# Kernel tuning notes

Measured on AMD Instinct MI355X. Metric: run time of the kernel, lower is better.

Reference implementation:

```python
import jax, jax.numpy as jnp
import numpy as np
from jax import lax

N_FFT = 2048
HOP = 512
N_ITER = 60
MOMENTUM = 0.99 / (1.0 + 0.99)  # torchaudio normalizes momentum/(1+momentum)
EPS = 1e-16
PAD = N_FFT // 2


def _hann(n):
    # periodic hann window, matches torch.hann_window(n)
    return 0.5 - 0.5 * jnp.cos(2.0 * jnp.pi * jnp.arange(n, dtype=jnp.float32) / n)


def _stft(x, window):
    # x: (B, L) real -> (B, F, T) complex. center=True, reflect pad, onesided, unnormalized.
    B, L = x.shape
    xp = jnp.pad(x, ((0, 0), (PAD, PAD)), mode='reflect')
    T = 1 + (L + 2 * PAD - N_FFT) // HOP
    idx = jnp.arange(T)[:, None] * HOP + jnp.arange(N_FFT)[None, :]  # (T, N)
    frames = xp[:, idx] * window  # (B, T, N)
    spec = jnp.fft.rfft(frames, axis=-1)  # (B, T, F)
    return jnp.swapaxes(spec, 1, 2)  # (B, F, T)


def _istft(spec, window):
    # spec: (B, F, T) complex -> (B, hop*(T-1)) real. Matches torch.istft(center=True).
    B, F, T = spec.shape
    frames = jnp.fft.irfft(jnp.swapaxes(spec, 1, 2), n=N_FFT, axis=-1) * window  # (B, T, N)
    L_pad = N_FFT + HOP * (T - 1)
    idx_flat = (jnp.arange(T)[:, None] * HOP + jnp.arange(N_FFT)[None, :]).reshape(-1)
    y = jnp.zeros((B, L_pad), frames.dtype).at[:, idx_flat].add(frames.reshape(B, -1))
    wsq = jnp.zeros((L_pad,), window.dtype).at[idx_flat].add(
        jnp.tile(window * window, T))
    y = y / jnp.where(wsq > 1e-11, wsq, 1.0)
    return y[:, PAD:L_pad - PAD]


def _griffin_lim(spec, window):
    # spec: (B, F, T) nonnegative magnitudes (power=1.0 so no pow needed)
    spec_c = spec.astype(jnp.complex64)
    angles0 = jnp.ones_like(spec_c)   # rand_init=False -> full of ones
    tprev0 = jnp.zeros_like(spec_c)

    def step(carry, _):
        angles, tprev = carry
        inv = _istft(spec_c * angles, window)
        rebuilt = _stft(inv, window)
        a = rebuilt - tprev * MOMENTUM
        a = a / (jnp.abs(a) + EPS)
        return (a, rebuilt), None

    (angles, _), _ = lax.scan(step, (angles0, tprev0), None, length=N_ITER)
    return _istft(spec_c * angles, window)


def setup_inputs() -> dict:
    key = jax.random.key(0)
    B, T, F = 4, 400, N_FFT // 2 + 1
    spectrogram = jax.random.uniform(key, (B, T, F), dtype=jnp.float32)
    return {"spectrogram": spectrogram}


def reference(spectrogram):
    window = _hann(N_FFT)
    spec = jnp.transpose(spectrogram, (0, 2, 1))  # (B, F, T)
    return _griffin_lim(spec, window)  # (B, HOP*(T-1))
```

## Files before the change

kernel.cpp:

```cpp
#include <hip/hip_runtime.h>
#include <math.h>

constexpr int BB   = 4;
constexpr int TT   = 400;
constexpr int FF   = 1025;
constexpr int NFFT = 2048;
constexpr int HOP  = 512;
constexpr int PADD = 1024;
constexpr int LL   = HOP * (TT - 1);
constexpr int LPAD = NFFT + HOP * (TT - 1);
constexpr int NITER = 60;
constexpr double MOM = 0.99 / 1.99;
constexpr double EPSV = 1e-16;
constexpr double DPI = 3.14159265358979323846;

constexpr size_t OFF_TW1024 = 0;
constexpr size_t OFF_TW2048 = 2048;
constexpr size_t OFF_TPR    = 4098;
constexpr size_t OFF_FRM    = 3284098;
constexpr size_t OFF_XP     = 6560898;
constexpr size_t OFF_WIN32  = 7386242;
constexpr size_t OFF_WSQ32  = 7387266;
constexpr size_t WS_DOUBLES = 7490434;

__device__ __forceinline__ double2 cmuld(double2 a, double2 b) {
    return make_double2(a.x * b.x - a.y * b.y, a.x * b.y + a.y * b.x);
}

__device__ __forceinline__ float np_cosf(float x) {
    const float rint_cvt = 0x1.800000p+23f;
    float qf = __builtin_fmaf(x, 0x1.45f306p-1f, rint_cvt) - rint_cvt;
    float r = __builtin_fmaf(qf, -0x1.921fb0p+0f, x);
    r = __builtin_fmaf(qf, -0x1.5110b4p-22f, r);
    r = __builtin_fmaf(qf, -0x1.846988p-48f, r);
    r = __builtin_fmaf(qf, -0x1.8cc966p-73f, r);
    int q = (int)qf + 1;
    float r2 = r * r;
    float cosp = __builtin_fmaf(0x1.98e616p-16f, r2, -0x1.6c06dcp-10f);
    cosp = __builtin_fmaf(cosp, r2, 0x1.55553cp-5f);
    cosp = __builtin_fmaf(cosp, r2, -0x1.000000p-1f);
    cosp = __builtin_fmaf(cosp, r2, 0x1.000000p+0f);
    float sinp = __builtin_fmaf(0x1.7d3bbcp-19f, r2, -0x1.a06bbap-13f);
    sinp = __builtin_fmaf(sinp, r2, 0x1.11119ap-7f);
    sinp = __builtin_fmaf(sinp, r2, -0x1.555548p-3f);
    sinp = sinp * r2;
    sinp = __builtin_fmaf(sinp, r, r);
    float res = (q & 1) ? cosp : sinp;
    return (q & 2) ? -res : res;
}

__global__ void k_init_tables(double2* tw1024, double2* tw2048, float* win) {
    int n = blockIdx.x * blockDim.x + threadIdx.x;
    if (n < 1024) {
        double th = -2.0 * DPI * (double)n / 1024.0;
        double s, c; sincos(th, &s, &c);
        tw1024[n] = make_double2(c, s);
    }
    if (n < 1025) {
        double th = -2.0 * DPI * (double)n / 2048.0;
        double s, c; sincos(th, &s, &c);
        tw2048[n] = make_double2(c, s);
    }
    if (n < 2048) {
        const float TWO_PI_F = 6.283185307179586f;
        float ang = __fdiv_rn(__fmul_rn(TWO_PI_F, (float)n), 2048.0f);
        float c = np_cosf(ang);
        win[n] = __fsub_rn(0.5f, __fmul_rn(0.5f, c));
    }
}

__global__ void k_init_wsq(const float* __restrict__ win, float* __restrict__ wsq) {
    int m = blockIdx.x * blockDim.x + threadIdx.x;
    if (m >= LPAD) return;
    int tlo = (m - (NFFT - HOP)) >> 9;
    if (tlo < 0) tlo = 0;
    int thi = m >> 9;
    if (thi > TT - 1) thi = TT - 1;
    float s = 0.0f;
    for (int t = tlo; t <= thi; ++t) {
        float w = win[m - (t << 9)];
        s = __fadd_rn(s, __fmul_rn(w, w));
    }
    wsq[m] = (s > 1e-11f) ? s : 1.0f;
}

__global__ void k_init_state(double2* __restrict__ tpr) {
    int i = blockIdx.x * blockDim.x + threadIdx.x;
    if (i < BB * TT * FF) tpr[i] = make_double2(0.0, 0.0);
}

template <int DIR>
__device__ void fft1024_w(double2* buf, const double2* __restrict__ tw, int tid) {
#pragma unroll
    for (int s = 0; s < 5; ++s) {
        const int p = 1 << (2 * s);
        double2 o0[4], o1[4], o2[4], o3[4];
        int jj[4];
#pragma unroll
        for (int q = 0; q < 4; ++q) {
            int v = tid + 64 * q;
            int k = v & (p - 1);
            jj[q] = ((v - k) << 2) + k;
            double2 a = buf[v];
            double2 b = buf[v + 256];
            double2 c = buf[v + 512];
            double2 d = buf[v + 768];
            int t1 = k << (8 - 2 * s);
            double2 w1 = tw[t1 & 1023];
            double2 w2 = tw[(2 * t1) & 1023];
            double2 w3 = tw[(3 * t1) & 1023];
            if (DIR > 0) { w1.y = -w1.y; w2.y = -w2.y; w3.y = -w3.y; }
            b = cmuld(b, w1);
            c = cmuld(c, w2);
            d = cmuld(d, w3);
            double2 u0 = make_double2(a.x + c.x, a.y + c.y);
            double2 u1 = make_double2(a.x - c.x, a.y - c.y);
            double2 v0 = make_double2(b.x + d.x, b.y + d.y);
            double2 v1 = make_double2(b.x - d.x, b.y - d.y);
            o0[q] = make_double2(u0.x + v0.x, u0.y + v0.y);
            o2[q] = make_double2(u0.x - v0.x, u0.y - v0.y);
            if (DIR < 0) {
                o1[q] = make_double2(u1.x + v1.y, u1.y - v1.x);
                o3[q] = make_double2(u1.x - v1.y, u1.y + v1.x);
            } else {
                o1[q] = make_double2(u1.x - v1.y, u1.y + v1.x);
                o3[q] = make_double2(u1.x + v1.y, u1.y - v1.x);
            }
        }
        __syncthreads();
#pragma unroll
        for (int q = 0; q < 4; ++q) {
            buf[jj[q]]         = o0[q];
            buf[jj[q] + p]     = o1[q];
            buf[jj[q] + 2 * p] = o2[q];
            buf[jj[q] + 3 * p] = o3[q];
        }
        __syncthreads();
    }
}

__device__ __forceinline__ double2 phase_step(double2 zk, double2 zc, double2 w,
                                              double2 tp, float mgf, double2* Xk_out) {
    zc.y = -zc.y;
    double2 A = make_double2(0.5 * (zk.x + zc.x), 0.5 * (zk.y + zc.y));
    double2 D = make_double2(zk.x - zc.x, zk.y - zc.y);
    double2 Bv = make_double2(0.5 * D.y, -0.5 * D.x);
    double2 wB = cmuld(w, Bv);
    double2 Xk = make_double2(A.x + wB.x, A.y + wB.y);
    double2 a = make_double2(Xk.x - MOM * tp.x, Xk.y - MOM * tp.y);
    double r = sqrt(a.x * a.x + a.y * a.y);
    double d = r + EPSV;
    *Xk_out = Xk;
    double m = (double)mgf;
    return make_double2(m * (a.x / d), m * (a.y / d));
}

__device__ __forceinline__ double2 pretwist(double2 Xk, double2 Xc, double2 w) {
    Xc.y = -Xc.y;
    double2 A = make_double2(0.5 * (Xk.x + Xc.x), 0.5 * (Xk.y + Xc.y));
    double2 D = make_double2(0.5 * (Xk.x - Xc.x), 0.5 * (Xk.y - Xc.y));
    w.y = -w.y;
    double2 Bv = cmuld(w, D);
    return make_double2(A.x - Bv.y, A.y + Bv.x);
}

__global__ __launch_bounds__(64) void k_istft_first(
    const float* __restrict__ mag,
    const double2* __restrict__ tw1024, const double2* __restrict__ tw2048,
    const float* __restrict__ win, double* __restrict__ frames_out) {
    __shared__ double2 S[1025];
    const int fid = blockIdx.x;
    const int tid = threadIdx.x;
    const float* mg = mag + (size_t)fid * FF;
#pragma unroll
    for (int q = 0; q < 8; ++q) {
        int k = tid + 64 * q;
        double mk = (double)mg[k];
        if (k == 0) {
            double m1024 = (double)mg[1024];
            double m512  = (double)mg[512];
            S[0]   = pretwist(make_double2(mk, 0.0),   make_double2(m1024, 0.0), tw2048[0]);
            S[512] = pretwist(make_double2(m512, 0.0), make_double2(m512, 0.0),  tw2048[512]);
        } else {
            int kp = 1024 - k;
            double mp = (double)mg[kp];
            S[k]  = pretwist(make_double2(mk, 0.0), make_double2(mp, 0.0), tw2048[k]);
            S[kp] = pretwist(make_double2(mp, 0.0), make_double2(mk, 0.0), tw2048[kp]);
        }
    }
    __syncthreads();
    fft1024_w<1>(S, tw1024, tid);
    double2* fr = reinterpret_cast<double2*>(frames_out + (size_t)fid * NFFT);
    const float2* w2 = reinterpret_cast<const float2*>(win);
#pragma unroll
    for (int q = 0; q < 16; ++q) {
        int m = tid + 64 * q;
        double2 z = S[m];
        float2 wv = w2[m];
        fr[m] = make_double2(z.x * (1.0 / 1024.0) * (double)wv.x,
                             z.y * (1.0 / 1024.0) * (double)wv.y);
    }
}

__global__ __launch_bounds__(256) void k_ola(
    const double* __restrict__ frames, const float* __restrict__ wsq,
    double* __restrict__ xp) {
    int gid = blockIdx.x * 256 + threadIdx.x;
    int b = gid / LPAD;
    int p = gid - b * LPAD;
    int j = p - PADD;
    if (j < 0) j = -j;
    else if (j >= LL) j = 2 * LL - 2 - j;
    int m = j + PADD;
    int tlo = (m - (NFFT - HOP)) >> 9;
    if (tlo < 0) tlo = 0;
    int thi = m >> 9;
    if (thi > TT - 1) thi = TT - 1;
    const double* fb = frames + (size_t)b * TT * NFFT;
    double s = 0.0;
    for (int t = tlo; t <= thi; ++t) s += fb[(size_t)t * NFFT + (m - (t << 9))];
    xp[gid] = s / (double)wsq[m];
}

__global__ __launch_bounds__(64) void k_fused(
    const double* __restrict__ xp, double* __restrict__ frames_out,
    const float* __restrict__ mag, double2* __restrict__ tpr,
    const double2* __restrict__ tw1024, const double2* __restrict__ tw2048,
    const float* __restrict__ win) {
    __shared__ double2 S[1025];
    const int fid = blockIdx.x;
    const int b = fid / TT;
    const int t = fid - b * TT;
    const int tid = threadIdx.x;
    const double2* xb = reinterpret_cast<const double2*>(xp + (size_t)b * LPAD + (size_t)t * HOP);
    const float2* w2 = reinterpret_cast<const float2*>(win);
#pragma unroll
    for (int q = 0; q < 16; ++q) {
        int k = tid + 64 * q;
        double2 v = xb[k];
        float2 wv = w2[k];
        S[k] = make_double2(v.x * (double)wv.x, v.y * (double)wv.y);
    }
    __syncthreads();
    fft1024_w<-1>(S, tw1024, tid);
    size_t base = (size_t)fid * FF;
    const float* mg = mag + base;
#pragma unroll
    for (int q = 0; q < 8; ++q) {
        int k = tid + 64 * q;
        int kp = 1024 - k;
        double2 zk = S[k];
        double2 zc = S[kp & 1023];
        double2 wk = tw2048[k];
        double2 Xk;
        double2 Snew_k = phase_step(zk, zc, wk, tpr[base + k], mg[k], &Xk);
        tpr[base + k] = Xk;
        if (k == 0) {
            double2 X1024;
            double2 Snew_1024 = phase_step(zk, zk, tw2048[1024], tpr[base + 1024], mg[1024], &X1024);
            tpr[base + 1024] = X1024;
            double2 z512 = S[512];
            double2 X512;
            double2 Snew_512 = phase_step(z512, z512, tw2048[512], tpr[base + 512], mg[512], &X512);
            tpr[base + 512] = X512;
            double2 Xk0 = Snew_k;   Xk0.y = 0.0;
            double2 Xc0 = Snew_1024; Xc0.y = 0.0;
            S[0]   = pretwist(Xk0, Xc0, tw2048[0]);
            S[512] = pretwist(Snew_512, Snew_512, tw2048[512]);
        } else {
            double2 wp = tw2048[kp];
            double2 Xp;
            double2 Snew_p = phase_step(zc, zk, wp, tpr[base + kp], mg[kp], &Xp);
            tpr[base + kp] = Xp;
            S[k]  = pretwist(Snew_k, Snew_p, wk);
            S[kp] = pretwist(Snew_p, Snew_k, wp);
        }
    }
    __syncthreads();
    fft1024_w<1>(S, tw1024, tid);
    double2* fr = reinterpret_cast<double2*>(frames_out + (size_t)fid * NFFT);
#pragma unroll
    for (int q = 0; q < 16; ++q) {
        int m = tid + 64 * q;
        double2 z = S[m];
        float2 wv = w2[m];
        fr[m] = make_double2(z.x * (1.0 / 1024.0) * (double)wv.x,
                             z.y * (1.0 / 1024.0) * (double)wv.y);
    }
}

__global__ __launch_bounds__(256) void k_ola_out(
    const double* __restrict__ frames, const float* __restrict__ wsq,
    float* __restrict__ out) {
    int gid = blockIdx.x * 256 + threadIdx.x;
    int b = gid / LL;
    int j = gid - b * LL;
    int m = j + PADD;
    int tlo = (m - (NFFT - HOP)) >> 9;
    if (tlo < 0) tlo = 0;
    int thi = m >> 9;
    if (thi > TT - 1) thi = TT - 1;
    const double* fb = frames + (size_t)b * TT * NFFT;
    double s = 0.0;
    for (int t = tlo; t <= thi; ++t) s += fb[(size_t)t * NFFT + (m - (t << 9))];
    out[gid] = (float)(s / (double)wsq[m]);
}

extern "C" void kernel_launch(void* const* d_in, const int* in_sizes, int n_in,
                              void* d_out, int out_size, void* d_ws, size_t ws_size,
                              hipStream_t stream) {
    if (ws_size < WS_DOUBLES * sizeof(double)) return;
    const float* mag = (const float*)d_in[0];
    double* ws = (double*)d_ws;
    double2* tw1024 = (double2*)(ws + OFF_TW1024);
    double2* tw2048 = (double2*)(ws + OFF_TW2048);
    double2* tprv   = (double2*)(ws + OFF_TPR);
    double* frames  = ws + OFF_FRM;
    double* xp      = ws + OFF_XP;
    float* win      = (float*)(ws + OFF_WIN32);
    float* wsq      = (float*)(ws + OFF_WSQ32);

    k_init_tables<<<8, 256, 0, stream>>>(tw1024, tw2048, win);
    k_init_wsq<<<LPAD / 256, 256, 0, stream>>>(win, wsq);
    k_init_state<<<(BB * TT * FF + 255) / 256, 256, 0, stream>>>(tprv);

    k_istft_first<<<BB * TT, 64, 0, stream>>>(mag, tw1024, tw2048, win, frames);
    for (int it = 0; it < NITER; ++it) {
        k_ola<<<(BB * LPAD) / 256, 256, 0, stream>>>(frames, wsq, xp);
        k_fused<<<BB * TT, 64, 0, stream>>>(xp, frames, mag, tprv,
                                            tw1024, tw2048, win);
    }
    k_ola_out<<<(BB * LL) / 256, 256, 0, stream>>>(frames, wsq, (float*)d_out);
}
```

Before: 2.165 ms.

## Remap block indices per XCD and prefetch phase state before the FFT

Block IDs in the frame and OLA kernels are remapped so that consecutive hardware block IDs, which are dispatched round-robin across the MI355X's 8 XCDs, go to contiguous chunks of work. The aim is for each XCD's L2 to hold neighbouring frames and samples that share overlapping data. The fused kernel also loads the previous rebuilt spectrum and magnitudes into registers before the forward FFT, hiding global latency behind FFT work. This raises register pressure, and the remap depends on the grid sizes dividing exactly by 8 (1600, 3224 and 3192 blocks).

Result: slower. 2.298 ms (+6.2%).

```diff
diff --git a/kernel.cpp b/kernel.cpp
--- a/kernel.cpp
+++ b/kernel.cpp
@@ -169,7 +169,8 @@
     const double2* __restrict__ tw1024, const double2* __restrict__ tw2048,
     const float* __restrict__ win, double* __restrict__ frames_out) {
     __shared__ double2 S[1025];
-    const int fid = blockIdx.x;
+    const int bx = blockIdx.x;
+    const int fid = (bx & 7) * 200 + (bx >> 3);
     const int tid = threadIdx.x;
     const float* mg = mag + (size_t)fid * FF;
 #pragma unroll
@@ -205,7 +206,9 @@
 __global__ __launch_bounds__(256) void k_ola(
     const double* __restrict__ frames, const float* __restrict__ wsq,
     double* __restrict__ xp) {
-    int gid = blockIdx.x * 256 + threadIdx.x;
+    int bx = blockIdx.x;
+    int bid = (bx & 7) * 403 + (bx >> 3);
+    int gid = bid * 256 + threadIdx.x;
     int b = gid / LPAD;
     int p = gid - b * LPAD;
     int j = p - PADD;
@@ -228,12 +231,31 @@
     const double2* __restrict__ tw1024, const double2* __restrict__ tw2048,
     const float* __restrict__ win) {
     __shared__ double2 S[1025];
-    const int fid = blockIdx.x;
+    const int bx = blockIdx.x;
+    const int fid = (bx & 7) * 200 + (bx >> 3);
     const int b = fid / TT;
     const int t = fid - b * TT;
     const int tid = threadIdx.x;
     const double2* xb = reinterpret_cast<const double2*>(xp + (size_t)b * LPAD + (size_t)t * HOP);
     const float2* w2 = reinterpret_cast<const float2*>(win);
+    size_t base = (size_t)fid * FF;
+    const float* mg = mag + base;
+    double2 tpk[8], tpp[8];
+    float mgk[8], mgp[8];
+    double2 tp512, tp1024; float mg512f, mg1024f;
+#pragma unroll
+    for (int q = 0; q < 8; ++q) {
+        int k = tid + 64 * q;
+        int kp = 1024 - k;
+        tpk[q] = tpr[base + k];
+        tpp[q] = tpr[base + kp];
+        mgk[q] = mg[k];
+        mgp[q] = mg[kp];
+    }
+    if (tid == 0) {
+        tp512  = tpr[base + 512];  mg512f  = mg[512];
+        tp1024 = tpp[0];           mg1024f = mgp[0];
+    }
 #pragma unroll
     for (int q = 0; q < 16; ++q) {
         int k = tid + 64 * q;
@@ -243,8 +265,6 @@
     }
     __syncthreads();
     fft1024_w<-1>(S, tw1024, tid);
-    size_t base = (size_t)fid * FF;
-    const float* mg = mag + base;
 #pragma unroll
     for (int q = 0; q < 8; ++q) {
         int k = tid + 64 * q;
@@ -253,15 +273,15 @@
         double2 zc = S[kp & 1023];
         double2 wk = tw2048[k];
         double2 Xk;
-        double2 Snew_k = phase_step(zk, zc, wk, tpr[base + k], mg[k], &Xk);
+        double2 Snew_k = phase_step(zk, zc, wk, tpk[q], mgk[q], &Xk);
         tpr[base + k] = Xk;
         if (k == 0) {
             double2 X1024;
-            double2 Snew_1024 = phase_step(zk, zk, tw2048[1024], tpr[base + 1024], mg[1024], &X1024);
+            double2 Snew_1024 = phase_step(zk, zk, tw2048[1024], tp1024, mg1024f, &X1024);
             tpr[base + 1024] = X1024;
             double2 z512 = S[512];
             double2 X512;
-            double2 Snew_512 = phase_step(z512, z512, tw2048[512], tpr[base + 512], mg[512], &X512);
+            double2 Snew_512 = phase_step(z512, z512, tw2048[512], tp512, mg512f, &X512);
             tpr[base + 512] = X512;
             double2 Xk0 = Snew_k;   Xk0.y = 0.0;
             double2 Xc0 = Snew_1024; Xc0.y = 0.0;
@@ -270,7 +290,7 @@
         } else {
             double2 wp = tw2048[kp];
             double2 Xp;
-            double2 Snew_p = phase_step(zc, zk, wp, tpr[base + kp], mg[kp], &Xp);
+            double2 Snew_p = phase_step(zc, zk, wp, tpp[q], mgp[q], &Xp);
             tpr[base + kp] = Xp;
             S[k]  = pretwist(Snew_k, Snew_p, wk);
             S[kp] = pretwist(Snew_p, Snew_k, wp);
@@ -292,7 +312,9 @@
 __global__ __launch_bounds__(256) void k_ola_out(
     const double* __restrict__ frames, const float* __restrict__ wsq,
     float* __restrict__ out) {
-    int gid = blockIdx.x * 256 + threadIdx.x;
+    int bx = blockIdx.x;
+    int bid = (bx & 7) * 399 + (bx >> 3);
+    int gid = bid * 256 + threadIdx.x;
     int b = gid / LL;
     int j = gid - b * LL;
     int m = j + PADD;
```

## Restructure fused-kernel FFT into register-resident radix-16 passes with swizzled LDS

Applied to the files above, without the earlier changes.

Replaces the five-stage shared-memory radix-4 FFT in the fused Griffin-Lim kernel with a register-based formulation. Each thread holds 16 values and does two radix-4 stages in registers per LDS exchange, so only two shared-memory transposes are needed. An XOR swizzle on LDS indices is meant to reduce bank conflicts. This cuts LDS traffic and barriers per FFT, at the cost of higher register pressure (16+ double2 per thread) that may lower occupancy.

After: 1.881 ms. -13.1%, faster.

```diff
diff --git a/kernel.cpp b/kernel.cpp
--- a/kernel.cpp
+++ b/kernel.cpp
@@ -26,6 +26,8 @@
 __device__ __forceinline__ double2 cmuld(double2 a, double2 b) {
     return make_double2(a.x * b.x - a.y * b.y, a.x * b.y + a.y * b.x);
 }
+
+__device__ __forceinline__ int swz(int f) { return f ^ ((f >> 4) & 7); }
 
 __device__ __forceinline__ float np_cosf(float x) {
     const float rint_cvt = 0x1.800000p+23f;
@@ -89,53 +91,90 @@
     if (i < BB * TT * FF) tpr[i] = make_double2(0.0, 0.0);
 }
 
+template <int DIR, bool TW>
+__device__ __forceinline__ void bfly4(double2 a, double2 b, double2 c, double2 d,
+                                      double2 w1, double2 w2, double2 w3,
+                                      double2& o0, double2& o1, double2& o2, double2& o3) {
+    if (TW) {
+        if (DIR > 0) { w1.y = -w1.y; w2.y = -w2.y; w3.y = -w3.y; }
+        b = cmuld(b, w1);
+        c = cmuld(c, w2);
+        d = cmuld(d, w3);
+    }
+    double2 u0 = make_double2(a.x + c.x, a.y + c.y);
+    double2 u1 = make_double2(a.x - c.x, a.y - c.y);
+    double2 v0 = make_double2(b.x + d.x, b.y + d.y);
+    double2 v1 = make_double2(b.x - d.x, b.y - d.y);
+    o0 = make_double2(u0.x + v0.x, u0.y + v0.y);
+    o2 = make_double2(u0.x - v0.x, u0.y - v0.y);
+    if (DIR < 0) {
+        o1 = make_double2(u1.x + v1.y, u1.y - v1.x);
+        o3 = make_double2(u1.x - v1.y, u1.y + v1.x);
+    } else {
+        o1 = make_double2(u1.x - v1.y, u1.y + v1.x);
+        o3 = make_double2(u1.x + v1.y, u1.y - v1.x);
+    }
+}
+
 template <int DIR>
-__device__ void fft1024_w(double2* buf, const double2* __restrict__ tw, int tid) {
-#pragma unroll
-    for (int s = 0; s < 5; ++s) {
-        const int p = 1 << (2 * s);
-        double2 o0[4], o1[4], o2[4], o3[4];
-        int jj[4];
-#pragma unroll
-        for (int q = 0; q < 4; ++q) {
-            int v = tid + 64 * q;
-            int k = v & (p - 1);
-            jj[q] = ((v - k) << 2) + k;
-            double2 a = buf[v];
-            double2 b = buf[v + 256];
-            double2 c = buf[v + 512];
-            double2 d = buf[v + 768];
-            int t1 = k << (8 - 2 * s);
-            double2 w1 = tw[t1 & 1023];
-            double2 w2 = tw[(2 * t1) & 1023];
-            double2 w3 = tw[(3 * t1) & 1023];
-            if (DIR > 0) { w1.y = -w1.y; w2.y = -w2.y; w3.y = -w3.y; }
-            b = cmuld(b, w1);
-            c = cmuld(c, w2);
-            d = cmuld(d, w3);
-            double2 u0 = make_double2(a.x + c.x, a.y + c.y);
-            double2 u1 = make_double2(a.x - c.x, a.y - c.y);
-            double2 v0 = make_double2(b.x + d.x, b.y + d.y);
-            double2 v1 = make_double2(b.x - d.x, b.y - d.y);
-            o0[q] = make_double2(u0.x + v0.x, u0.y + v0.y);
-            o2[q] = make_double2(u0.x - v0.x, u0.y - v0.y);
-            if (DIR < 0) {
-                o1[q] = make_double2(u1.x + v1.y, u1.y - v1.x);
-                o3[q] = make_double2(u1.x - v1.y, u1.y + v1.x);
-            } else {
-                o1[q] = make_double2(u1.x - v1.y, u1.y + v1.x);
-                o3[q] = make_double2(u1.x + v1.y, u1.y - v1.x);
-            }
-        }
-        __syncthreads();
-#pragma unroll
-        for (int q = 0; q < 4; ++q) {
-            buf[jj[q]]         = o0[q];
-            buf[jj[q] + p]     = o1[q];
-            buf[jj[q] + 2 * p] = o2[q];
-            buf[jj[q] + 3 * p] = o3[q];
-        }
-        __syncthreads();
+__device__ void fft1024_reg(double2 r[16], double2* S, const double2* __restrict__ tw, int tid) {
+    const double2 wid = make_double2(1.0, 0.0);
+    double2 e[4][4];
+#pragma unroll
+    for (int m = 0; m < 4; ++m)
+        bfly4<DIR, false>(r[m], r[m + 4], r[m + 8], r[m + 12], wid, wid, wid,
+                          e[m][0], e[m][1], e[m][2], e[m][3]);
+    double2 g[4][4];
+#pragma unroll
+    for (int r1 = 0; r1 < 4; ++r1) {
+        int t1 = r1 << 6;
+        bfly4<DIR, true>(e[0][r1], e[1][r1], e[2][r1], e[3][r1],
+                         tw[t1 & 1023], tw[(2 * t1) & 1023], tw[(3 * t1) & 1023],
+                         g[r1][0], g[r1][1], g[r1][2], g[r1][3]);
+    }
+#pragma unroll
+    for (int r1 = 0; r1 < 4; ++r1)
+#pragma unroll
+        for (int u = 0; u < 4; ++u)
+            S[swz(16 * tid + r1 + 4 * u)] = g[r1][u];
+    __syncthreads();
+    double2 r2[16];
+#pragma unroll
+    for (int j = 0; j < 16; ++j) r2[j] = S[swz(tid + 64 * j)];
+    const int kapp = tid & 15;
+    const int aa = tid >> 4;
+    double2 h[4][4];
+    {
+        int t = kapp << 4;
+        double2 w1 = tw[t & 1023], w2 = tw[(2 * t) & 1023], w3 = tw[(3 * t) & 1023];
+#pragma unroll
+        for (int m = 0; m < 4; ++m)
+            bfly4<DIR, true>(r2[m], r2[m + 4], r2[m + 8], r2[m + 12], w1, w2, w3,
+                             h[m][0], h[m][1], h[m][2], h[m][3]);
+    }
+    double2 gg[4][4];
+#pragma unroll
+    for (int u = 0; u < 4; ++u) {
+        int t = (kapp + 16 * u) << 2;
+        bfly4<DIR, true>(h[0][u], h[1][u], h[2][u], h[3][u],
+                         tw[t & 1023], tw[(2 * t) & 1023], tw[(3 * t) & 1023],
+                         gg[u][0], gg[u][1], gg[u][2], gg[u][3]);
+    }
+#pragma unroll
+    for (int u = 0; u < 4; ++u)
+#pragma unroll
+        for (int w = 0; w < 4; ++w)
+            S[swz(256 * aa + kapp + 16 * u + 64 * w)] = gg[u][w];
+    __syncthreads();
+    double2 r4[16];
+#pragma unroll
+    for (int j = 0; j < 16; ++j) r4[j] = S[swz(tid + 64 * j)];
+#pragma unroll
+    for (int m = 0; m < 4; ++m) {
+        int t = tid + 64 * m;
+        bfly4<DIR, true>(r4[m], r4[m + 4], r4[m + 8], r4[m + 12],
+                         tw[t & 1023], tw[(2 * t) & 1023], tw[(3 * t) & 1023],
+                         r[m], r[m + 4], r[m + 8], r[m + 12]);
     }
 }
 
@@ -162,6 +201,39 @@
     w.y = -w.y;
     double2 Bv = cmuld(w, D);
     return make_double2(A.x - Bv.y, A.y + Bv.x);
+}
+
+template <int DIR>
+__device__ void fft1024_w(double2* buf, const double2* __restrict__ tw, int tid) {
+#pragma unroll
+    for (int s = 0; s < 5; ++s) {
+        const int p = 1 << (2 * s);
+        double2 o0[4], o1[4], o2[4], o3[4];
+        int jj[4];
+#pragma unroll
+        for (int q = 0; q < 4; ++q) {
+            int v = tid + 64 * q;
+            int k = v & (p - 1);
+            jj[q] = ((v - k) << 2) + k;
+            double2 a = buf[v];
+            double2 b = buf[v + 256];
+            double2 c = buf[v + 512];
+            double2 d = buf[v + 768];
+            int t1 = k << (8 - 2 * s);
+            bfly4<DIR, true>(a, b, c, d,
+                             tw[t1 & 1023], tw[(2 * t1) & 1023], tw[(3 * t1) & 1023],
+                             o0[q], o1[q], o2[q], o3[q]);
+        }
+        __syncthreads();
+#pragma unroll
+        for (int q = 0; q < 4; ++q) {
+            buf[jj[q]]         = o0[q];
+            buf[jj[q] + p]     = o1[q];
+            buf[jj[q] + 2 * p] = o2[q];
+            buf[jj[q] + 3 * p] = o3[q];
+        }
+        __syncthreads();
+    }
 }
 
 __global__ __launch_bounds__(64) void k_istft_first(
@@ -227,30 +299,33 @@
     const float* __restrict__ mag, double2* __restrict__ tpr,
     const double2* __restrict__ tw1024, const double2* __restrict__ tw2048,
     const float* __restrict__ win) {
-    __shared__ double2 S[1025];
+    __shared__ double2 S[1024];
     const int fid = blockIdx.x;
     const int b = fid / TT;
     const int t = fid - b * TT;
     const int tid = threadIdx.x;
     const double2* xb = reinterpret_cast<const double2*>(xp + (size_t)b * LPAD + (size_t)t * HOP);
     const float2* w2 = reinterpret_cast<const float2*>(win);
-#pragma unroll
-    for (int q = 0; q < 16; ++q) {
-        int k = tid + 64 * q;
+    double2 r[16];
+#pragma unroll
+    for (int j = 0; j < 16; ++j) {
+        int k = tid + 64 * j;
         double2 v = xb[k];
         float2 wv = w2[k];
-        S[k] = make_double2(v.x * (double)wv.x, v.y * (double)wv.y);
-    }
+        r[j] = make_double2(v.x * (double)wv.x, v.y * (double)wv.y);
+    }
+    fft1024_reg<-1>(r, S, tw1024, tid);
+#pragma unroll
+    for (int j = 0; j < 16; ++j) S[swz(tid + 64 * j)] = r[j];
     __syncthreads();
-    fft1024_w<-1>(S, tw1024, tid);
     size_t base = (size_t)fid * FF;
     const float* mg = mag + base;
 #pragma unroll
     for (int q = 0; q < 8; ++q) {
         int k = tid + 64 * q;
         int kp = 1024 - k;
-        double2 zk = S[k];
-        double2 zc = S[kp & 1023];
+        double2 zk = S[swz(k)];
+        double2 zc = S[swz(kp & 1023)];
         double2 wk = tw2048[k];
         double2 Xk;
         double2 Snew_k = phase_step(zk, zc, wk, tpr[base + k], mg[k], &Xk);
@@ -259,33 +334,34 @@
             double2 X1024;
             double2 Snew_1024 = phase_step(zk, zk, tw2048[1024], tpr[base + 1024], mg[1024], &X1024);
             tpr[base + 1024] = X1024;
-            double2 z512 = S[512];
+            double2 z512 = S[swz(512)];
             double2 X512;
             double2 Snew_512 = phase_step(z512, z512, tw2048[512], tpr[base + 512], mg[512], &X512);
             tpr[base + 512] = X512;
-            double2 Xk0 = Snew_k;   Xk0.y = 0.0;
+            double2 Xk0 = Snew_k;    Xk0.y = 0.0;
             double2 Xc0 = Snew_1024; Xc0.y = 0.0;
-            S[0]   = pretwist(Xk0, Xc0, tw2048[0]);
-            S[512] = pretwist(Snew_512, Snew_512, tw2048[512]);
+            S[swz(0)]   = pretwist(Xk0, Xc0, tw2048[0]);
+            S[swz(512)] = pretwist(Snew_512, Snew_512, tw2048[512]);
         } else {
             double2 wp = tw2048[kp];
             double2 Xp;
             double2 Snew_p = phase_step(zc, zk, wp, tpr[base + kp], mg[kp], &Xp);
             tpr[base + kp] = Xp;
-            S[k]  = pretwist(Snew_k, Snew_p, wk);
-            S[kp] = pretwist(Snew_p, Snew_k, wp);
+            S[swz(k)]  = pretwist(Snew_k, Snew_p, wk);
+            S[swz(kp)] = pretwist(Snew_p, Snew_k, wp);
         }
     }
     __syncthreads();
-    fft1024_w<1>(S, tw1024, tid);
+#pragma unroll
+    for (int j = 0; j < 16; ++j) r[j] = S[swz(tid + 64 * j)];
+    fft1024_reg<1>(r, S, tw1024, tid);
     double2* fr = reinterpret_cast<double2*>(frames_out + (size_t)fid * NFFT);
 #pragma unroll
-    for (int q = 0; q < 16; ++q) {
-        int m = tid + 64 * q;
-        double2 z = S[m];
+    for (int j = 0; j < 16; ++j) {
+        int m = tid + 64 * j;
         float2 wv = w2[m];
-        fr[m] = make_double2(z.x * (1.0 / 1024.0) * (double)wv.x,
-                             z.y * (1.0 / 1024.0) * (double)wv.y);
+        fr[m] = make_double2(r[j].x * (1.0 / 1024.0) * (double)wv.x,
+                             r[j].y * (1.0 / 1024.0) * (double)wv.y);
     }
 }
 
```

## Ping-pong swizzled LDS FFT with 128 threads and XCD-aware block remapping

Applied to the files above, without the earlier changes.

The fused STFT/phase/ISTFT kernel now uses 128 threads per frame instead of 64. Its radix-4 FFT ping-pongs between two LDS buffers, which drops one barrier per stage, and the LDS indices are XOR-swizzled to reduce bank conflicts. Block IDs in the fused and overlap-add kernels are remapped so that neighbouring work is grouped per XCD, aiming for better L2 locality. The cost is double the LDS per block (32KB), which may lower occupancy.

Result: slower. 2.229 ms (+3.0%).

```diff
diff --git a/kernel.cpp b/kernel.cpp
--- a/kernel.cpp
+++ b/kernel.cpp
@@ -26,6 +26,8 @@
 __device__ __forceinline__ double2 cmuld(double2 a, double2 b) {
     return make_double2(a.x * b.x - a.y * b.y, a.x * b.y + a.y * b.x);
 }
+
+__device__ __forceinline__ int swz(int f) { return f ^ ((f >> 4) & 7); }
 
 __device__ __forceinline__ float np_cosf(float x) {
     const float rint_cvt = 0x1.800000p+23f;
@@ -89,53 +91,59 @@
     if (i < BB * TT * FF) tpr[i] = make_double2(0.0, 0.0);
 }
 
+template <int DIR, bool TW>
+__device__ __forceinline__ void bfly4(double2 a, double2 b, double2 c, double2 d,
+                                      double2 w1, double2 w2, double2 w3,
+                                      double2& o0, double2& o1, double2& o2, double2& o3) {
+    if (TW) {
+        if (DIR > 0) { w1.y = -w1.y; w2.y = -w2.y; w3.y = -w3.y; }
+        b = cmuld(b, w1);
+        c = cmuld(c, w2);
+        d = cmuld(d, w3);
+    }
+    double2 u0 = make_double2(a.x + c.x, a.y + c.y);
+    double2 u1 = make_double2(a.x - c.x, a.y - c.y);
+    double2 v0 = make_double2(b.x + d.x, b.y + d.y);
+    double2 v1 = make_double2(b.x - d.x, b.y - d.y);
+    o0 = make_double2(u0.x + v0.x, u0.y + v0.y);
+    o2 = make_double2(u0.x - v0.x, u0.y - v0.y);
+    if (DIR < 0) {
+        o1 = make_double2(u1.x + v1.y, u1.y - v1.x);
+        o3 = make_double2(u1.x - v1.y, u1.y + v1.x);
+    } else {
+        o1 = make_double2(u1.x - v1.y, u1.y + v1.x);
+        o3 = make_double2(u1.x + v1.y, u1.y - v1.x);
+    }
+}
+
 template <int DIR>
-__device__ void fft1024_w(double2* buf, const double2* __restrict__ tw, int tid) {
+__device__ void fft1024_st(double2* SA, double2* SB, const double2* __restrict__ tw, int tau) {
+    double2* src = SA;
+    double2* dst = SB;
 #pragma unroll
     for (int s = 0; s < 5; ++s) {
         const int p = 1 << (2 * s);
-        double2 o0[4], o1[4], o2[4], o3[4];
-        int jj[4];
-#pragma unroll
-        for (int q = 0; q < 4; ++q) {
-            int v = tid + 64 * q;
+        double2 o0[2], o1[2], o2[2], o3[2];
+        int jj[2];
+#pragma unroll
+        for (int m = 0; m < 2; ++m) {
+            int v = tau + 128 * m;
             int k = v & (p - 1);
-            jj[q] = ((v - k) << 2) + k;
-            double2 a = buf[v];
-            double2 b = buf[v + 256];
-            double2 c = buf[v + 512];
-            double2 d = buf[v + 768];
+            jj[m] = ((v - k) << 2) + k;
             int t1 = k << (8 - 2 * s);
-            double2 w1 = tw[t1 & 1023];
-            double2 w2 = tw[(2 * t1) & 1023];
-            double2 w3 = tw[(3 * t1) & 1023];
-            if (DIR > 0) { w1.y = -w1.y; w2.y = -w2.y; w3.y = -w3.y; }
-            b = cmuld(b, w1);
-            c = cmuld(c, w2);
-            d = cmuld(d, w3);
-            double2 u0 = make_double2(a.x + c.x, a.y + c.y);
-            double2 u1 = make_double2(a.x - c.x, a.y - c.y);
-            double2 v0 = make_double2(b.x + d.x, b.y + d.y);
-            double2 v1 = make_double2(b.x - d.x, b.y - d.y);
-            o0[q] = make_double2(u0.x + v0.x, u0.y + v0.y);
-            o2[q] = make_double2(u0.x - v0.x, u0.y - v0.y);
-            if (DIR < 0) {
-                o1[q] = make_double2(u1.x + v1.y, u1.y - v1.x);
-                o3[q] = make_double2(u1.x - v1.y, u1.y + v1.x);
-            } else {
-                o1[q] = make_double2(u1.x - v1.y, u1.y + v1.x);
-                o3[q] = make_double2(u1.x + v1.y, u1.y - v1.x);
-            }
+            bfly4<DIR, true>(src[swz(v)], src[swz(v + 256)], src[swz(v + 512)], src[swz(v + 768)],
+                             tw[t1 & 1023], tw[(2 * t1) & 1023], tw[(3 * t1) & 1023],
+                             o0[m], o1[m], o2[m], o3[m]);
+        }
+#pragma unroll
+        for (int m = 0; m < 2; ++m) {
+            dst[swz(jj[m])]         = o0[m];
+            dst[swz(jj[m] + p)]     = o1[m];
+            dst[swz(jj[m] + 2 * p)] = o2[m];
+            dst[swz(jj[m] + 3 * p)] = o3[m];
         }
         __syncthreads();
-#pragma unroll
-        for (int q = 0; q < 4; ++q) {
-            buf[jj[q]]         = o0[q];
-            buf[jj[q] + p]     = o1[q];
-            buf[jj[q] + 2 * p] = o2[q];
-            buf[jj[q] + 3 * p] = o3[q];
-        }
-        __syncthreads();
+        double2* tmp = src; src = dst; dst = tmp;
     }
 }
 
@@ -164,6 +172,35 @@
     return make_double2(A.x - Bv.y, A.y + Bv.x);
 }
 
+template <int DIR>
+__device__ void fft1024_w(double2* buf, const double2* __restrict__ tw, int tid) {
+#pragma unroll
+    for (int s = 0; s < 5; ++s) {
+        const int p = 1 << (2 * s);
+        double2 o0[4], o1[4], o2[4], o3[4];
+        int jj[4];
+#pragma unroll
+        for (int q = 0; q < 4; ++q) {
+            int v = tid + 64 * q;
+            int k = v & (p - 1);
+            jj[q] = ((v - k) << 2) + k;
+            int t1 = k << (8 - 2 * s);
+            bfly4<DIR, true>(buf[v], buf[v + 256], buf[v + 512], buf[v + 768],
+                             tw[t1 & 1023], tw[(2 * t1) & 1023], tw[(3 * t1) & 1023],
+                             o0[q], o1[q], o2[q], o3[q]);
+        }
+        __syncthreads();
+#pragma unroll
+        for (int q = 0; q < 4; ++q) {
+            buf[jj[q]]         = o0[q];
+            buf[jj[q] + p]     = o1[q];
+            buf[jj[q] + 2 * p] = o2[q];
+            buf[jj[q] + 3 * p] = o3[q];
+        }
+        __syncthreads();
+    }
+}
+
 __global__ __launch_bounds__(64) void k_istft_first(
     const float* __restrict__ mag,
     const double2* __restrict__ tw1024, const double2* __restrict__ tw2048,
@@ -205,7 +242,9 @@
 __global__ __launch_bounds__(256) void k_ola(
     const double* __restrict__ frames, const float* __restrict__ wsq,
     double* __restrict__ xp) {
-    int gid = blockIdx.x * 256 + threadIdx.x;
+    int bx = blockIdx.x;
+    int bid = (bx & 7) * 403 + (bx >> 3);
+    int gid = bid * 256 + threadIdx.x;
     int b = gid / LPAD;
     int p = gid - b * LPAD;
     int j = p - PADD;
@@ -222,35 +261,37 @@
     xp[gid] = s / (double)wsq[m];
 }
 
-__global__ __launch_bounds__(64) void k_fused(
+__global__ __launch_bounds__(128) void k_fused(
     const double* __restrict__ xp, double* __restrict__ frames_out,
     const float* __restrict__ mag, double2* __restrict__ tpr,
     const double2* __restrict__ tw1024, const double2* __restrict__ tw2048,
     const float* __restrict__ win) {
-    __shared__ double2 S[1025];
-    const int fid = blockIdx.x;
+    __shared__ double2 SA[1024];
+    __shared__ double2 SB[1024];
+    const int bx = blockIdx.x;
+    const int fid = (bx & 7) * 200 + (bx >> 3);
     const int b = fid / TT;
     const int t = fid - b * TT;
-    const int tid = threadIdx.x;
+    const int tau = threadIdx.x;
     const double2* xb = reinterpret_cast<const double2*>(xp + (size_t)b * LPAD + (size_t)t * HOP);
     const float2* w2 = reinterpret_cast<const float2*>(win);
 #pragma unroll
-    for (int q = 0; q < 16; ++q) {
-        int k = tid + 64 * q;
+    for (int j = 0; j < 8; ++j) {
+        int k = tau + 128 * j;
         double2 v = xb[k];
         float2 wv = w2[k];
-        S[k] = make_double2(v.x * (double)wv.x, v.y * (double)wv.y);
+        SA[swz(k)] = make_double2(v.x * (double)wv.x, v.y * (double)wv.y);
     }
     __syncthreads();
-    fft1024_w<-1>(S, tw1024, tid);
+    fft1024_st<-1>(SA, SB, tw1024, tau);
     size_t base = (size_t)fid * FF;
     const float* mg = mag + base;
 #pragma unroll
-    for (int q = 0; q < 8; ++q) {
-        int k = tid + 64 * q;
+    for (int q = 0; q < 4; ++q) {
+        int k = tau + 128 * q;
         int kp = 1024 - k;
-        double2 zk = S[k];
-        double2 zc = S[kp & 1023];
+        double2 zk = SB[swz(k)];
+        double2 zc = SB[swz(kp & 1023)];
         double2 wk = tw2048[k];
         double2 Xk;
         double2 Snew_k = phase_step(zk, zc, wk, tpr[base + k], mg[k], &Xk);
@@ -259,30 +300,30 @@
             double2 X1024;
             double2 Snew_1024 = phase_step(zk, zk, tw2048[1024], tpr[base + 1024], mg[1024], &X1024);
             tpr[base + 1024] = X1024;
-            double2 z512 = S[512];
+            double2 z512 = SB[swz(512)];
             double2 X512;
             double2 Snew_512 = phase_step(z512, z512, tw2048[512], tpr[base + 512], mg[512], &X512);
             tpr[base + 512] = X512;
-            double2 Xk0 = Snew_k;   Xk0.y = 0.0;
+            double2 Xk0 = Snew_k;    Xk0.y = 0.0;
             double2 Xc0 = Snew_1024; Xc0.y = 0.0;
-            S[0]   = pretwist(Xk0, Xc0, tw2048[0]);
-            S[512] = pretwist(Snew_512, Snew_512, tw2048[512]);
+            SA[swz(0)]   = pretwist(Xk0, Xc0, tw2048[0]);
+            SA[swz(512)] = pretwist(Snew_512, Snew_512, tw2048[512]);
         } else {
             double2 wp = tw2048[kp];
             double2 Xp;
             double2 Snew_p = phase_step(zc, zk, wp, tpr[base + kp], mg[kp], &Xp);
             tpr[base + kp] = Xp;
-            S[k]  = pretwist(Snew_k, Snew_p, wk);
-            S[kp] = pretwist(Snew_p, Snew_k, wp);
+            SA[swz(k)]  = pretwist(Snew_k, Snew_p, wk);
+            SA[swz(kp)] = pretwist(Snew_p, Snew_k, wp);
         }
     }
     __syncthreads();
-    fft1024_w<1>(S, tw1024, tid);
+    fft1024_st<1>(SA, SB, tw1024, tau);
     double2* fr = reinterpret_cast<double2*>(frames_out + (size_t)fid * NFFT);
 #pragma unroll
-    for (int q = 0; q < 16; ++q) {
-        int m = tid + 64 * q;
-        double2 z = S[m];
+    for (int j = 0; j < 8; ++j) {
+        int m = tau + 128 * j;
+        double2 z = SB[swz(m)];
         float2 wv = w2[m];
         fr[m] = make_double2(z.x * (1.0 / 1024.0) * (double)wv.x,
                              z.y * (1.0 / 1024.0) * (double)wv.y);
@@ -292,7 +333,9 @@
 __global__ __launch_bounds__(256) void k_ola_out(
     const double* __restrict__ frames, const float* __restrict__ wsq,
     float* __restrict__ out) {
-    int gid = blockIdx.x * 256 + threadIdx.x;
+    int bx = blockIdx.x;
+    int bid = (bx & 7) * 399 + (bx >> 3);
+    int gid = bid * 256 + threadIdx.x;
     int b = gid / LL;
     int j = gid - b * LL;
     int m = j + PADD;
@@ -327,8 +370,8 @@
     k_istft_first<<<BB * TT, 64, 0, stream>>>(mag, tw1024, tw2048, win, frames);
     for (int it = 0; it < NITER; ++it) {
         k_ola<<<(BB * LPAD) / 256, 256, 0, stream>>>(frames, wsq, xp);
-        k_fused<<<BB * TT, 64, 0, stream>>>(xp, frames, mag, tprv,
-                                            tw1024, tw2048, win);
+        k_fused<<<BB * TT, 128, 0, stream>>>(xp, frames, mag, tprv,
+                                             tw1024, tw2048, win);
     }
     k_ola_out<<<(BB * LL) / 256, 256, 0, stream>>>(frames, wsq, (float*)d_out);
 }
```
